# Performance work log

Hardware: AMD Instinct MI355X
Metric: run time of the kernel (lower is better)

Reference implementation:

```python
import jax, jax.numpy as jnp
import numpy as np

AREA = 4
HEADS = 8

def conv1x1(x, W, b):
    # x: [B,C,H,W], W: [O,C], b: [O]
    return jnp.einsum('bchw,oc->bohw', x, W) + b[None, :, None, None]

def dwconv5(x, W, b):
    # depthwise 5x5, pad 2, groups = C; W: [C,1,5,5]
    C = x.shape[1]
    y = jax.lax.conv_general_dilated(
        x, W, window_strides=(1, 1), padding=[(2, 2), (2, 2)],
        dimension_numbers=('NCHW', 'OIHW', 'NCHW'), feature_group_count=C)
    return y + b[None, :, None, None]

def setup_inputs() -> dict:
    key = jax.random.key(0)
    ks = jax.random.split(key, 9)
    B, C, H, W = 4, 256, 64, 64
    s = 0.05
    return {
        'x': jax.random.normal(ks[0], (B, C, H, W), jnp.float32),
        'Wqk': jax.random.normal(ks[1], (2 * C, C), jnp.float32) * s,
        'bqk': jax.random.normal(ks[2], (2 * C,), jnp.float32) * s,
        'Wv': jax.random.normal(ks[3], (C, C), jnp.float32) * s,
        'bv': jax.random.normal(ks[4], (C,), jnp.float32) * s,
        'Wpe': jax.random.normal(ks[5], (C, 1, 5, 5), jnp.float32) * s,
        'bpe': jax.random.normal(ks[6], (C,), jnp.float32) * s,
        'Wproj': jax.random.normal(ks[7], (C, C), jnp.float32) * s,
        'bproj': jax.random.normal(ks[8], (C,), jnp.float32) * s,
    }

def reference(x, Wqk, bqk, Wv, bv, Wpe, bpe, Wproj, bproj):
    B, C, H, W = x.shape
    N = H * W
    hd = C // HEADS
    # qk / v projections (1x1 conv + folded BN bias, no activation)
    qk = conv1x1(x, Wqk, bqk).reshape(B, 2 * C, N).transpose(0, 2, 1)  # [B,N,2C]
    v4 = conv1x1(x, Wv, bv)                                            # [B,C,H,W]
    pp = dwconv5(v4, Wpe, bpe)                                         # positional enc
    v = v4.reshape(B, C, N).transpose(0, 2, 1)                         # [B,N,C]
    # area split: [B*area, N/area, .]
    Ba, Na = B * AREA, N // AREA
    qk = qk.reshape(Ba, Na, 2 * C)
    v = v.reshape(Ba, Na, C)
    q, k = qk[..., :C], qk[..., C:]
    q = q.reshape(Ba, Na, HEADS, hd)
    k = k.reshape(Ba, Na, HEADS, hd)
    v = v.reshape(Ba, Na, HEADS, hd)
    # manual softmax attention: (q^T k) * d^-0.5 -> softmax -> weight v
    attn = jnp.einsum('bqhd,bkhd->bhqk', q, k) * (hd ** -0.5)
    attn = jax.nn.softmax(attn, axis=-1)
    out = jnp.einsum('bhqk,bkhd->bqhd', attn, v)                       # [Ba,Na,H,hd]
    # merge areas back and go to NCHW
    out = out.reshape(B, N, C).reshape(B, H, W, C).transpose(0, 3, 1, 2)
    return conv1x1(out + pp, Wproj, bproj)
```

## Files before the change

kernel.cpp:

```cpp
#include <hip/hip_runtime.h>

typedef unsigned short u16;
typedef unsigned int u32;
using f32x4  = __attribute__((ext_vector_type(4))) float;
using u32x2  = __attribute__((ext_vector_type(2))) u32;
using u32x4  = __attribute__((ext_vector_type(4))) u32;
using bf16x8 = __attribute__((ext_vector_type(8))) short;

__device__ __forceinline__ u16 f2b(float f) {
  union { float f; u32 u; } v; v.f = f;
  return (u16)((v.u + 0x7FFFu + ((v.u >> 16) & 1u)) >> 16);
}
__device__ __forceinline__ float b2f(u16 u) {
  union { u32 u; float f; } v; v.u = ((u32)u) << 16;
  return v.f;
}
__device__ __forceinline__ u32 pk2(float a, float b) {
  u32 r;
  asm("v_cvt_pk_bf16_f32 %0, %1, %2" : "=v"(r) : "v"(a), "v"(b));
  return r;
}

__global__ __launch_bounds__(256) void kconvert(
    const float* __restrict__ Wqk, const float* __restrict__ Wv,
    const float* __restrict__ Wproj, u16* __restrict__ dst) {
  int e = (blockIdx.x * 256 + threadIdx.x) * 4;
  f32x4 v;
  if (e < 131072)      v = *(const f32x4*)(Wqk + e);
  else if (e < 196608) v = *(const f32x4*)(Wv + (e - 131072));
  else                 v = *(const f32x4*)(Wproj + (e - 196608));
  u32* d = (u32*)(dst + e);
  d[0] = (u32)f2b(v[0]) | ((u32)f2b(v[1]) << 16);
  d[1] = (u32)f2b(v[2]) | ((u32)f2b(v[3]) << 16);
}

__global__ __launch_bounds__(512) void kqkv(
    const float* __restrict__ x,
    const u16* __restrict__ Wqk_bf, const float* __restrict__ bqk,
    const u16* __restrict__ Wv_bf,  const float* __restrict__ bv,
    u16* __restrict__ qk_tm, u16* __restrict__ v_cm) {
  __shared__ __align__(16) u16 xs[64 * 264];
  const int bid = blockIdx.x;
  const int b   = bid >> 6;
  const int n0  = (bid & 63) * 64;
  const int tid = threadIdx.x;

  {
    const int part = tid & 15, cr = tid >> 4;
    #pragma unroll
    for (int p = 0; p < 8; ++p) {
      const int c = p * 32 + cr;
      f32x4 v = *(const f32x4*)(x + (size_t)(b * 256 + c) * 4096 + n0 + part * 4);
      const int t0 = part * 4;
      xs[(t0 + 0) * 264 + c] = f2b(v[0]);
      xs[(t0 + 1) * 264 + c] = f2b(v[1]);
      xs[(t0 + 2) * 264 + c] = f2b(v[2]);
      xs[(t0 + 3) * 264 + c] = f2b(v[3]);
    }
  }
  __syncthreads();

  const int wave = tid >> 6, l = tid & 63, lg = l & 15, lq = l >> 4;
  const float kscale = 0.25503484f;

  for (int ot = wave; ot < 48; ot += 8) {
    if (ot < 32) {
      bf16x8 bfr[8];
      const u16* wrow = Wqk_bf + (ot * 16 + lg) * 256 + lq * 8;
      #pragma unroll
      for (int kk = 0; kk < 8; ++kk) bfr[kk] = *(const bf16x8*)(wrow + kk * 32);
      const float bias = bqk[ot * 16 + lg];
      const float scl  = (ot >= 16) ? kscale : 1.0f;
      #pragma unroll
      for (int ts = 0; ts < 4; ++ts) {
        f32x4 acc = {0.f, 0.f, 0.f, 0.f};
        #pragma unroll
        for (int kk = 0; kk < 8; ++kk) {
          bf16x8 af = *(const bf16x8*)(&xs[(ts * 16 + lg) * 264 + kk * 32 + lq * 8]);
          acc = __builtin_amdgcn_mfma_f32_16x16x32_bf16(af, bfr[kk], acc, 0, 0, 0);
        }
        u16* dst = qk_tm + (size_t)(b * 4096 + n0 + ts * 16 + lq * 4) * 512 + ot * 16 + lg;
        #pragma unroll
        for (int r = 0; r < 4; ++r) dst[(size_t)r * 512] = f2b((acc[r] + bias) * scl);
      }
    } else {
      const int o2 = ot - 32;
      bf16x8 afw[8];
      const u16* wrow = Wv_bf + (o2 * 16 + lg) * 256 + lq * 8;
      #pragma unroll
      for (int kk = 0; kk < 8; ++kk) afw[kk] = *(const bf16x8*)(wrow + kk * 32);
      float bvr[4];
      #pragma unroll
      for (int r = 0; r < 4; ++r) bvr[r] = bv[o2 * 16 + lq * 4 + r];
      #pragma unroll
      for (int ts = 0; ts < 4; ++ts) {
        f32x4 acc = {0.f, 0.f, 0.f, 0.f};
        #pragma unroll
        for (int kk = 0; kk < 8; ++kk) {
          bf16x8 bfx = *(const bf16x8*)(&xs[(ts * 16 + lg) * 264 + kk * 32 + lq * 8]);
          acc = __builtin_amdgcn_mfma_f32_16x16x32_bf16(afw[kk], bfx, acc, 0, 0, 0);
        }
        #pragma unroll
        for (int r = 0; r < 4; ++r) {
          const int o = o2 * 16 + lq * 4 + r;
          v_cm[(size_t)(b * 256 + o) * 4096 + n0 + ts * 16 + lg] = f2b(acc[r] + bvr[r]);
        }
      }
    }
  }
}

__global__ __launch_bounds__(256) void kdw(
    const u16* __restrict__ v_cm, const float* __restrict__ Wpe,
    const float* __restrict__ bpe, u16* __restrict__ pp) {
  __shared__ __align__(16) u16 vsh[5 * 64 * 64];
  __shared__ float wsh[64 * 25];
  const int bid = blockIdx.x;
  const int ct = bid & 3, h = (bid >> 2) & 63, b = bid >> 8;
  const int c0 = ct * 64;
  const int tid = threadIdx.x;

  for (int i = tid; i < 64 * 25; i += 256) wsh[i] = Wpe[(c0 + i / 25) * 25 + i % 25];
  #pragma unroll
  for (int uu = 0; uu < 10; ++uu) {
    const int u = uu * 256 + tid;
    const int dy = u >> 9, rem = u & 511, c = rem >> 3, part = rem & 7;
    const int hy = h + dy - 2;
    u32x4 val = {0, 0, 0, 0};
    if (hy >= 0 && hy < 64)
      val = *(const u32x4*)(v_cm + (size_t)(b * 256 + c0 + c) * 4096 + hy * 64 + part * 8);
    *(u32x4*)(&vsh[(dy * 64 + c) * 64 + part * 8]) = val;
  }
  __syncthreads();

  const int c = tid >> 2, w0 = (tid & 3) * 16;
  float acc16[16];
  const float bias = bpe[c0 + c];
  #pragma unroll
  for (int i = 0; i < 16; ++i) acc16[i] = bias;
  const float* wc = &wsh[c * 25];
  #pragma unroll
  for (int dy = 0; dy < 5; ++dy) {
    const u16* row = &vsh[(dy * 64 + c) * 64];
    float rowv[20];
    #pragma unroll
    for (int j = 0; j < 20; ++j) {
      const int ww = w0 + j - 2;
      rowv[j] = (ww >= 0 && ww < 64) ? b2f(row[ww]) : 0.f;
    }
    #pragma unroll
    for (int dx = 0; dx < 5; ++dx) {
      const float wv = wc[dy * 5 + dx];
      #pragma unroll
      for (int wi = 0; wi < 16; ++wi) acc16[wi] += rowv[wi + dx] * wv;
    }
  }
  u32x4 o0, o1;
  #pragma unroll
  for (int i = 0; i < 4; ++i)
    o0[i] = (u32)f2b(acc16[2 * i]) | ((u32)f2b(acc16[2 * i + 1]) << 16);
  #pragma unroll
  for (int i = 0; i < 4; ++i)
    o1[i] = (u32)f2b(acc16[8 + 2 * i]) | ((u32)f2b(acc16[9 + 2 * i]) << 16);
  u16* dst = pp + (size_t)(b * 256 + c0 + c) * 4096 + h * 64 + w0;
  *(u32x4*)(dst) = o0;
  *(u32x4*)(dst + 8) = o1;
}

__global__ __launch_bounds__(256) void kattn(
    const u16* __restrict__ qk_tm, const u16* __restrict__ v_cm,
    u16* __restrict__ out_tm) {
  __shared__ __align__(16) char pbuf[4][32 * 128];

  const int bid = blockIdx.x;
  const int xcd = bid & 7, idx = bid >> 3;
  const int pair = xcd * 16 + (idx >> 3);
  const int qb = idx & 7;
  const int h = pair & 7, ba = pair >> 3;
  const int b = ba >> 2, area = ba & 3;
  const size_t row_base = (size_t)b * 4096 + area * 1024;

  const int tid = threadIdx.x;
  const int wave = tid >> 6, l = tid & 63, lg = l & 15, lq = l >> 4;
  char* pbc = pbuf[wave];
  const int swz = (lg & 7) << 4;

  bf16x8 bQ[2];
  #pragma unroll
  for (int s = 0; s < 2; ++s) {
    const size_t qrow = row_base + qb * 128 + wave * 32 + s * 16 + lg;
    bQ[s] = *(const bf16x8*)(qk_tm + qrow * 512 + h * 32 + lq * 8);
  }

  const u16* Kbase = qk_tm + row_base * 512 + 256 + h * 32 + lq * 8;
  const u16* Vbase = v_cm + (size_t)(b * 256 + h * 32) * 4096 + area * 1024 + lq * 8;

  f32x4 accO[2][2];
  float dAcc[2] = {0.f, 0.f};
  #pragma unroll
  for (int s = 0; s < 2; ++s)
    #pragma unroll
    for (int d = 0; d < 2; ++d) accO[s][d] = (f32x4){0.f, 0.f, 0.f, 0.f};

  bf16x8 fK0[4], fV0[4], fK1[4], fV1[4];

  auto LOAD = [&](bf16x8* fK, bf16x8* fV, int kb) {
    #pragma unroll
    for (int t = 0; t < 4; ++t)
      fK[t] = *(const bf16x8*)(Kbase + (size_t)(kb * 64 + t * 16 + lg) * 512);
    #pragma unroll
    for (int kk = 0; kk < 2; ++kk)
      #pragma unroll
      for (int dt = 0; dt < 2; ++dt)
        fV[kk * 2 + dt] = *(const bf16x8*)(Vbase + (size_t)(dt * 16 + lg) * 4096 + kb * 64 + kk * 32);
  };

  auto COMP = [&](bf16x8* fK, bf16x8* fV) {
    f32x4 sc[2][4];
    #pragma unroll
    for (int s = 0; s < 2; ++s)
      #pragma unroll
      for (int t = 0; t < 4; ++t) {
        f32x4 z = {0.f, 0.f, 0.f, 0.f};
        sc[s][t] = __builtin_amdgcn_mfma_f32_16x16x32_bf16(fK[t], bQ[s], z, 0, 0, 0);
      }
    #pragma unroll
    for (int s = 0; s < 2; ++s)
      #pragma unroll
      for (int t = 0; t < 4; ++t) {
        const float e0 = __builtin_amdgcn_exp2f(sc[s][t][0]);
        const float e1 = __builtin_amdgcn_exp2f(sc[s][t][1]);
        const float e2 = __builtin_amdgcn_exp2f(sc[s][t][2]);
        const float e3 = __builtin_amdgcn_exp2f(sc[s][t][3]);
        dAcc[s] += (e0 + e1) + (e2 + e3);
        u32x2 w = {pk2(e0, e1), pk2(e2, e3)};
        *(u32x2*)(pbc + (s * 16 + lg) * 128 + ((t * 32 + lq * 8) ^ swz)) = w;
      }
    asm volatile("s_waitcnt lgkmcnt(0)" ::: "memory");
    __builtin_amdgcn_sched_barrier(0);
    #pragma unroll
    for (int s = 0; s < 2; ++s)
      #pragma unroll
      for (int kk = 0; kk < 2; ++kk) {
        bf16x8 aP = *(const bf16x8*)(pbc + (s * 16 + lg) * 128 + ((kk * 64 + lq * 16) ^ swz));
        #pragma unroll
        for (int dt = 0; dt < 2; ++dt)
          accO[s][dt] = __builtin_amdgcn_mfma_f32_16x16x32_bf16(aP, fV[kk * 2 + dt], accO[s][dt], 0, 0, 0);
      }
  };

  LOAD(fK0, fV0, 0);
  for (int kb = 0; kb < 16; kb += 2) {
    LOAD(fK1, fV1, kb + 1);
    COMP(fK0, fV0);
    if (kb + 2 < 16) LOAD(fK0, fV0, kb + 2);
    COMP(fK1, fV1);
  }

  #pragma unroll
  for (int s = 0; s < 2; ++s) {
    float d = dAcc[s];
    d += __shfl_xor(d, 16);
    d += __shfl_xor(d, 32);
    #pragma unroll
    for (int r = 0; r < 4; ++r) {
      const float den = __shfl(d, lq * 4 + r);
      const float inv = __builtin_amdgcn_rcpf(den);
      const size_t row = row_base + qb * 128 + wave * 32 + s * 16 + lq * 4 + r;
      u16* dst = out_tm + row * 256 + h * 32 + lg;
      dst[0]  = f2b(accO[s][0][r] * inv);
      dst[16] = f2b(accO[s][1][r] * inv);
    }
  }
}

__global__ __launch_bounds__(512) void kproj(
    const u16* __restrict__ out_tm, const u16* __restrict__ pp,
    const u16* __restrict__ Wproj_bf, const float* __restrict__ bproj,
    float* __restrict__ out) {
  __shared__ __align__(16) u16 as_[64 * 264];
  const int bid = blockIdx.x;
  const int b = bid >> 6;
  const int n0 = (bid & 63) * 64;
  const int tid = threadIdx.x;
  {
    const int r = tid >> 3, qp = tid & 7;
    const u32x4* src = (const u32x4*)(out_tm + (size_t)(b * 4096 + n0 + r) * 256 + qp * 32);
    #pragma unroll
    for (int j = 0; j < 4; ++j)
      *(u32x4*)(&as_[r * 264 + qp * 32 + j * 8]) = src[j];
  }
  __syncthreads();
  {
    const int part = tid & 7;
    #pragma unroll
    for (int pass = 0; pass < 4; ++pass) {
      const int c = pass * 64 + (tid >> 3);
      u32x4 v = *(const u32x4*)(pp + (size_t)(b * 256 + c) * 4096 + n0 + part * 8);
      #pragma unroll
      for (int jj = 0; jj < 4; ++jj) {
        u32 w = v[jj];
        u16* q0 = &as_[(part * 8 + jj * 2) * 264 + c];
        *q0 = f2b(b2f(*q0) + b2f((u16)(w & 0xffffu)));
        u16* q1 = &as_[(part * 8 + jj * 2 + 1) * 264 + c];
        *q1 = f2b(b2f(*q1) + b2f((u16)(w >> 16)));
      }
    }
  }
  __syncthreads();
  const int wave = tid >> 6, l = tid & 63, lg = l & 15, lq = l >> 4;
  #pragma unroll
  for (int oi = 0; oi < 2; ++oi) {
    const int ot = oi * 8 + wave;
    bf16x8 afw[8];
    const u16* wrow = Wproj_bf + (ot * 16 + lg) * 256 + lq * 8;
    #pragma unroll
    for (int kk = 0; kk < 8; ++kk) afw[kk] = *(const bf16x8*)(wrow + kk * 32);
    float bpr[4];
    #pragma unroll
    for (int r = 0; r < 4; ++r) bpr[r] = bproj[ot * 16 + lq * 4 + r];
    #pragma unroll
    for (int ts = 0; ts < 4; ++ts) {
      f32x4 acc = {0.f, 0.f, 0.f, 0.f};
      #pragma unroll
      for (int kk = 0; kk < 8; ++kk) {
        bf16x8 bfx = *(const bf16x8*)(&as_[(ts * 16 + lg) * 264 + kk * 32 + lq * 8]);
        acc = __builtin_amdgcn_mfma_f32_16x16x32_bf16(afw[kk], bfx, acc, 0, 0, 0);
      }
      #pragma unroll
      for (int r = 0; r < 4; ++r) {
        const int o = ot * 16 + lq * 4 + r;
        out[(size_t)(b * 256 + o) * 4096 + n0 + ts * 16 + lg] = acc[r] + bpr[r];
      }
    }
  }
}

extern "C" void kernel_launch(void* const* d_in, const int* in_sizes, int n_in,
                              void* d_out, int out_size, void* d_ws, size_t ws_size,
                              hipStream_t stream) {
  const float* x     = (const float*)d_in[0];
  const float* Wqk   = (const float*)d_in[1];
  const float* bqk   = (const float*)d_in[2];
  const float* Wv    = (const float*)d_in[3];
  const float* bv    = (const float*)d_in[4];
  const float* Wpe   = (const float*)d_in[5];
  const float* bpe   = (const float*)d_in[6];
  const float* Wproj = (const float*)d_in[7];
  const float* bproj = (const float*)d_in[8];
  float* out = (float*)d_out;

  char* ws = (char*)d_ws;
  u16* qk_tm  = (u16*)(ws);
  u16* v_cm   = (u16*)(ws + 16777216);
  u16* pp     = (u16*)(ws + 25165824);
  u16* out_tm = (u16*)(ws + 33554432);
  u16* wbf    = (u16*)(ws + 41943040);
  u16* Wqk_bf = wbf;
  u16* Wv_bf = wbf + 131072;
  u16* Wproj_bf = wbf + 196608;

  kconvert<<<256, 256, 0, stream>>>(Wqk, Wv, Wproj, wbf);
  kqkv<<<256, 512, 0, stream>>>(x, Wqk_bf, bqk, Wv_bf, bv, qk_tm, v_cm);
  kdw<<<1024, 256, 0, stream>>>(v_cm, Wpe, bpe, pp);
  kattn<<<1024, 256, 0, stream>>>(qk_tm, v_cm, out_tm);
  kproj<<<256, 512, 0, stream>>>(out_tm, pp, Wproj_bf, bproj, out);
}
```

Before: 123.0 us.

## Merge depthwise conv into attention launch as extra blocks with finer tiling

Folds the depthwise 5x5 positional-encoding kernel into the attention kernel as 4096 extra thread blocks, so both independent stages share one launch and can overlap on the GPU. The dwconv blocks are retiled to 16 channels per block with 4 outputs per thread, which cuts shared memory per block so it fits in the attention kernel's 16KB buffer and raises occupancy. This removes one kernel launch and its serialization gap. The cost is more redundant halo loads per output and a heterogeneous grid whose block mix can hurt scheduling balance.

```diff
diff --git a/kernel.cpp b/kernel.cpp
--- a/kernel.cpp
+++ b/kernel.cpp
@@ -110,167 +110,162 @@
   }
 }
 
-__global__ __launch_bounds__(256) void kdw(
-    const u16* __restrict__ v_cm, const float* __restrict__ Wpe,
-    const float* __restrict__ bpe, u16* __restrict__ pp) {
-  __shared__ __align__(16) u16 vsh[5 * 64 * 64];
-  __shared__ float wsh[64 * 25];
+__global__ __launch_bounds__(256) void kattn_dw(
+    const u16* __restrict__ qk_tm, const u16* __restrict__ v_cm,
+    const float* __restrict__ Wpe, const float* __restrict__ bpe,
+    u16* __restrict__ out_tm, u16* __restrict__ pp) {
+  __shared__ __align__(16) char smem[16384];
   const int bid = blockIdx.x;
-  const int ct = bid & 3, h = (bid >> 2) & 63, b = bid >> 8;
-  const int c0 = ct * 64;
   const int tid = threadIdx.x;
 
-  for (int i = tid; i < 64 * 25; i += 256) wsh[i] = Wpe[(c0 + i / 25) * 25 + i % 25];
-  #pragma unroll
-  for (int uu = 0; uu < 10; ++uu) {
-    const int u = uu * 256 + tid;
-    const int dy = u >> 9, rem = u & 511, c = rem >> 3, part = rem & 7;
-    const int hy = h + dy - 2;
-    u32x4 val = {0, 0, 0, 0};
-    if (hy >= 0 && hy < 64)
-      val = *(const u32x4*)(v_cm + (size_t)(b * 256 + c0 + c) * 4096 + hy * 64 + part * 8);
-    *(u32x4*)(&vsh[(dy * 64 + c) * 64 + part * 8]) = val;
-  }
-  __syncthreads();
-
-  const int c = tid >> 2, w0 = (tid & 3) * 16;
-  float acc16[16];
-  const float bias = bpe[c0 + c];
-  #pragma unroll
-  for (int i = 0; i < 16; ++i) acc16[i] = bias;
-  const float* wc = &wsh[c * 25];
-  #pragma unroll
-  for (int dy = 0; dy < 5; ++dy) {
-    const u16* row = &vsh[(dy * 64 + c) * 64];
-    float rowv[20];
-    #pragma unroll
-    for (int j = 0; j < 20; ++j) {
-      const int ww = w0 + j - 2;
-      rowv[j] = (ww >= 0 && ww < 64) ? b2f(row[ww]) : 0.f;
-    }
-    #pragma unroll
-    for (int dx = 0; dx < 5; ++dx) {
-      const float wv = wc[dy * 5 + dx];
-      #pragma unroll
-      for (int wi = 0; wi < 16; ++wi) acc16[wi] += rowv[wi + dx] * wv;
-    }
-  }
-  u32x4 o0, o1;
-  #pragma unroll
-  for (int i = 0; i < 4; ++i)
-    o0[i] = (u32)f2b(acc16[2 * i]) | ((u32)f2b(acc16[2 * i + 1]) << 16);
-  #pragma unroll
-  for (int i = 0; i < 4; ++i)
-    o1[i] = (u32)f2b(acc16[8 + 2 * i]) | ((u32)f2b(acc16[9 + 2 * i]) << 16);
-  u16* dst = pp + (size_t)(b * 256 + c0 + c) * 4096 + h * 64 + w0;
-  *(u32x4*)(dst) = o0;
-  *(u32x4*)(dst + 8) = o1;
-}
-
-__global__ __launch_bounds__(256) void kattn(
-    const u16* __restrict__ qk_tm, const u16* __restrict__ v_cm,
-    u16* __restrict__ out_tm) {
-  __shared__ __align__(16) char pbuf[4][32 * 128];
-
-  const int bid = blockIdx.x;
-  const int xcd = bid & 7, idx = bid >> 3;
-  const int pair = xcd * 16 + (idx >> 3);
-  const int qb = idx & 7;
-  const int h = pair & 7, ba = pair >> 3;
-  const int b = ba >> 2, area = ba & 3;
-  const size_t row_base = (size_t)b * 4096 + area * 1024;
-
-  const int tid = threadIdx.x;
-  const int wave = tid >> 6, l = tid & 63, lg = l & 15, lq = l >> 4;
-  char* pbc = pbuf[wave];
-  const int swz = (lg & 7) << 4;
-
-  bf16x8 bQ[2];
-  #pragma unroll
-  for (int s = 0; s < 2; ++s) {
-    const size_t qrow = row_base + qb * 128 + wave * 32 + s * 16 + lg;
-    bQ[s] = *(const bf16x8*)(qk_tm + qrow * 512 + h * 32 + lq * 8);
-  }
-
-  const u16* Kbase = qk_tm + row_base * 512 + 256 + h * 32 + lq * 8;
-  const u16* Vbase = v_cm + (size_t)(b * 256 + h * 32) * 4096 + area * 1024 + lq * 8;
-
-  f32x4 accO[2][2];
-  float dAcc[2] = {0.f, 0.f};
-  #pragma unroll
-  for (int s = 0; s < 2; ++s)
-    #pragma unroll
-    for (int d = 0; d < 2; ++d) accO[s][d] = (f32x4){0.f, 0.f, 0.f, 0.f};
-
-  bf16x8 fK0[4], fV0[4], fK1[4], fV1[4];
-
-  auto LOAD = [&](bf16x8* fK, bf16x8* fV, int kb) {
-    #pragma unroll
-    for (int t = 0; t < 4; ++t)
-      fK[t] = *(const bf16x8*)(Kbase + (size_t)(kb * 64 + t * 16 + lg) * 512);
-    #pragma unroll
-    for (int kk = 0; kk < 2; ++kk)
-      #pragma unroll
-      for (int dt = 0; dt < 2; ++dt)
-        fV[kk * 2 + dt] = *(const bf16x8*)(Vbase + (size_t)(dt * 16 + lg) * 4096 + kb * 64 + kk * 32);
-  };
-
-  auto COMP = [&](bf16x8* fK, bf16x8* fV) {
-    f32x4 sc[2][4];
+  if (bid < 1024) {
+    const int xcd = bid & 7, idx = bid >> 3;
+    const int pair = xcd * 16 + (idx >> 3);
+    const int qb = idx & 7;
+    const int h = pair & 7, ba = pair >> 3;
+    const int b = ba >> 2, area = ba & 3;
+    const size_t row_base = (size_t)b * 4096 + area * 1024;
+
+    const int wave = tid >> 6, l = tid & 63, lg = l & 15, lq = l >> 4;
+    char* pbc = smem + wave * 4096;
+    const int swz = (lg & 7) << 4;
+
+    bf16x8 bQ[2];
+    #pragma unroll
+    for (int s = 0; s < 2; ++s) {
+      const size_t qrow = row_base + qb * 128 + wave * 32 + s * 16 + lg;
+      bQ[s] = *(const bf16x8*)(qk_tm + qrow * 512 + h * 32 + lq * 8);
+    }
+
+    const u16* Kbase = qk_tm + row_base * 512 + 256 + h * 32 + lq * 8;
+    const u16* Vbase = v_cm + (size_t)(b * 256 + h * 32) * 4096 + area * 1024 + lq * 8;
+
+    f32x4 accO[2][2];
+    float dAcc[2] = {0.f, 0.f};
     #pragma unroll
     for (int s = 0; s < 2; ++s)
       #pragma unroll
-      for (int t = 0; t < 4; ++t) {
-        f32x4 z = {0.f, 0.f, 0.f, 0.f};
-        sc[s][t] = __builtin_amdgcn_mfma_f32_16x16x32_bf16(fK[t], bQ[s], z, 0, 0, 0);
-      }
-    #pragma unroll
-    for (int s = 0; s < 2; ++s)
-      #pragma unroll
-      for (int t = 0; t < 4; ++t) {
-        const float e0 = __builtin_amdgcn_exp2f(sc[s][t][0]);
-        const float e1 = __builtin_amdgcn_exp2f(sc[s][t][1]);
-        const float e2 = __builtin_amdgcn_exp2f(sc[s][t][2]);
-        const float e3 = __builtin_amdgcn_exp2f(sc[s][t][3]);
-        dAcc[s] += (e0 + e1) + (e2 + e3);
-        u32x2 w = {pk2(e0, e1), pk2(e2, e3)};
-        *(u32x2*)(pbc + (s * 16 + lg) * 128 + ((t * 32 + lq * 8) ^ swz)) = w;
-      }
-    asm volatile("s_waitcnt lgkmcnt(0)" ::: "memory");
-    __builtin_amdgcn_sched_barrier(0);
-    #pragma unroll
-    for (int s = 0; s < 2; ++s)
-      #pragma unroll
-      for (int kk = 0; kk < 2; ++kk) {
-        bf16x8 aP = *(const bf16x8*)(pbc + (s * 16 + lg) * 128 + ((kk * 64 + lq * 16) ^ swz));
+      for (int d = 0; d < 2; ++d) accO[s][d] = (f32x4){0.f, 0.f, 0.f, 0.f};
+
+    bf16x8 fK0[4], fV0[4], fK1[4], fV1[4];
+
+    auto LOAD = [&](bf16x8* fK, bf16x8* fV, int kb) {
+      #pragma unroll
+      for (int t = 0; t < 4; ++t)
+        fK[t] = *(const bf16x8*)(Kbase + (size_t)(kb * 64 + t * 16 + lg) * 512);
+      #pragma unroll
+      for (int kk = 0; kk < 2; ++kk)
         #pragma unroll
         for (int dt = 0; dt < 2; ++dt)
-          accO[s][dt] = __builtin_amdgcn_mfma_f32_16x16x32_bf16(aP, fV[kk * 2 + dt], accO[s][dt], 0, 0, 0);
-      }
-  };
-
-  LOAD(fK0, fV0, 0);
-  for (int kb = 0; kb < 16; kb += 2) {
-    LOAD(fK1, fV1, kb + 1);
-    COMP(fK0, fV0);
-    if (kb + 2 < 16) LOAD(fK0, fV0, kb + 2);
-    COMP(fK1, fV1);
-  }
-
-  #pragma unroll
-  for (int s = 0; s < 2; ++s) {
-    float d = dAcc[s];
-    d += __shfl_xor(d, 16);
-    d += __shfl_xor(d, 32);
-    #pragma unroll
-    for (int r = 0; r < 4; ++r) {
-      const float den = __shfl(d, lq * 4 + r);
-      const float inv = __builtin_amdgcn_rcpf(den);
-      const size_t row = row_base + qb * 128 + wave * 32 + s * 16 + lq * 4 + r;
-      u16* dst = out_tm + row * 256 + h * 32 + lg;
-      dst[0]  = f2b(accO[s][0][r] * inv);
-      dst[16] = f2b(accO[s][1][r] * inv);
-    }
+          fV[kk * 2 + dt] = *(const bf16x8*)(Vbase + (size_t)(dt * 16 + lg) * 4096 + kb * 64 + kk * 32);
+    };
+
+    auto COMP = [&](bf16x8* fK, bf16x8* fV) {
+      f32x4 sc[2][4];
+      #pragma unroll
+      for (int s = 0; s < 2; ++s)
+        #pragma unroll
+        for (int t = 0; t < 4; ++t) {
+          f32x4 z = {0.f, 0.f, 0.f, 0.f};
+          sc[s][t] = __builtin_amdgcn_mfma_f32_16x16x32_bf16(fK[t], bQ[s], z, 0, 0, 0);
+        }
+      #pragma unroll
+      for (int s = 0; s < 2; ++s)
+        #pragma unroll
+        for (int t = 0; t < 4; ++t) {
+          const float e0 = __builtin_amdgcn_exp2f(sc[s][t][0]);
+          const float e1 = __builtin_amdgcn_exp2f(sc[s][t][1]);
+          const float e2 = __builtin_amdgcn_exp2f(sc[s][t][2]);
+          const float e3 = __builtin_amdgcn_exp2f(sc[s][t][3]);
+          dAcc[s] += (e0 + e1) + (e2 + e3);
+          u32x2 w = {pk2(e0, e1), pk2(e2, e3)};
+          *(u32x2*)(pbc + (s * 16 + lg) * 128 + ((t * 32 + lq * 8) ^ swz)) = w;
+        }
+      asm volatile("s_waitcnt lgkmcnt(0)" ::: "memory");
+      __builtin_amdgcn_sched_barrier(0);
+      #pragma unroll
+      for (int s = 0; s < 2; ++s)
+        #pragma unroll
+        for (int kk = 0; kk < 2; ++kk) {
+          bf16x8 aP = *(const bf16x8*)(pbc + (s * 16 + lg) * 128 + ((kk * 64 + lq * 16) ^ swz));
+          #pragma unroll
+          for (int dt = 0; dt < 2; ++dt)
+            accO[s][dt] = __builtin_amdgcn_mfma_f32_16x16x32_bf16(aP, fV[kk * 2 + dt], accO[s][dt], 0, 0, 0);
+        }
+    };
+
+    LOAD(fK0, fV0, 0);
+    for (int kb = 0; kb < 16; kb += 2) {
+      LOAD(fK1, fV1, kb + 1);
+      COMP(fK0, fV0);
+      if (kb + 2 < 16) LOAD(fK0, fV0, kb + 2);
+      COMP(fK1, fV1);
+    }
+
+    #pragma unroll
+    for (int s = 0; s < 2; ++s) {
+      float d = dAcc[s];
+      d += __shfl_xor(d, 16);
+      d += __shfl_xor(d, 32);
+      #pragma unroll
+      for (int r = 0; r < 4; ++r) {
+        const float den = __shfl(d, lq * 4 + r);
+        const float inv = __builtin_amdgcn_rcpf(den);
+        const size_t row = row_base + qb * 128 + wave * 32 + s * 16 + lq * 4 + r;
+        u16* dst = out_tm + row * 256 + h * 32 + lg;
+        dst[0]  = f2b(accO[s][0][r] * inv);
+        dst[16] = f2b(accO[s][1][r] * inv);
+      }
+    }
+  } else {
+    const int kbid = bid - 1024;
+    const int ct = kbid & 15, h = (kbid >> 4) & 63, b = kbid >> 10;
+    const int c0 = ct * 16;
+    u16* vsh = (u16*)smem;
+    float* wsh = (float*)(smem + 10240);
+
+    for (int i = tid; i < 400; i += 256) wsh[i] = Wpe[(c0 + i / 25) * 25 + i % 25];
+    #pragma unroll
+    for (int uu = 0; uu < 3; ++uu) {
+      const int u = uu * 256 + tid;
+      if (u < 640) {
+        const int dy = u >> 7, rem = u & 127, c = rem >> 3, part = rem & 7;
+        const int hy = h + dy - 2;
+        u32x4 val = {0, 0, 0, 0};
+        if (hy >= 0 && hy < 64)
+          val = *(const u32x4*)(v_cm + (size_t)(b * 256 + c0 + c) * 4096 + hy * 64 + part * 8);
+        *(u32x4*)(&vsh[(dy * 16 + c) * 64 + part * 8]) = val;
+      }
+    }
+    __syncthreads();
+
+    const int c = tid >> 4, w0 = (tid & 15) * 4;
+    float acc4[4];
+    const float bias = bpe[c0 + c];
+    #pragma unroll
+    for (int i = 0; i < 4; ++i) acc4[i] = bias;
+    const float* wc = &wsh[c * 25];
+    #pragma unroll
+    for (int dy = 0; dy < 5; ++dy) {
+      const u16* row = &vsh[(dy * 16 + c) * 64];
+      float rowv[8];
+      #pragma unroll
+      for (int j = 0; j < 8; ++j) {
+        const int ww = w0 + j - 2;
+        rowv[j] = (ww >= 0 && ww < 64) ? b2f(row[ww]) : 0.f;
+      }
+      #pragma unroll
+      for (int dx = 0; dx < 5; ++dx) {
+        const float wv = wc[dy * 5 + dx];
+        #pragma unroll
+        for (int wi = 0; wi < 4; ++wi) acc4[wi] += rowv[wi + dx] * wv;
+      }
+    }
+    u32x2 o;
+    o[0] = (u32)f2b(acc4[0]) | ((u32)f2b(acc4[1]) << 16);
+    o[1] = (u32)f2b(acc4[2]) | ((u32)f2b(acc4[3]) << 16);
+    u16* dst = pp + (size_t)(b * 256 + c0 + c) * 4096 + h * 64 + w0;
+    *(u32x2*)(dst) = o;
   }
 }
 
@@ -362,7 +357,6 @@
 
   kconvert<<<256, 256, 0, stream>>>(Wqk, Wv, Wproj, wbf);
   kqkv<<<256, 512, 0, stream>>>(x, Wqk_bf, bqk, Wv_bf, bv, qk_tm, v_cm);
-  kdw<<<1024, 256, 0, stream>>>(v_cm, Wpe, bpe, pp);
-  kattn<<<1024, 256, 0, stream>>>(qk_tm, v_cm, out_tm);
+  kattn_dw<<<5120, 256, 0, stream>>>(qk_tm, v_cm, Wpe, bpe, out_tm, pp);
   kproj<<<256, 512, 0, stream>>>(out_tm, pp, Wproj_bf, bproj, out);
 }
```

Measured after the change: 124.6 us. Within noise of the previous version (+1.3%).
